# Kernel optimization log

Hardware: AMD Instinct MI355X
Metric: run time of the kernel (lower is better)

Reference implementation:

```python
import jax, jax.numpy as jnp
import numpy as np

VOCAB, X, H, C_CLS = 32000, 300, 512, 5
B, N_LEAVES = 256, 256  # complete binary trees, depth 9, 511 nodes/tree

def setup_inputs() -> dict:
    key = jax.random.key(0)
    ks = jax.random.split(key, 10)
    s = lambda k, shp, fan: jax.random.normal(k, shp, jnp.float32) * (1.0 / np.sqrt(fan))
    return {
        'wordid': jax.random.randint(ks[0], (B, N_LEAVES), 0, VOCAB),
        'emb': jax.random.normal(ks[1], (VOCAB, X), jnp.float32) * 0.1,
        'W_iou_w': s(ks[2], (3 * H, X), X),
        'W_iou_b': jnp.zeros((3 * H,), jnp.float32),
        'U_iou_w': s(ks[3], (3 * H, 2 * H), 2 * H),
        'U_iou_b': jnp.zeros((3 * H,), jnp.float32),
        'U_f_w': s(ks[4], (2 * H, 2 * H), 2 * H),
        'U_f_b': jnp.zeros((2 * H,), jnp.float32),
        'lin_w': s(ks[5], (C_CLS, H), H),
        'lin_b': jnp.zeros((C_CLS,), jnp.float32),
    }

def _cell(iou, c_f):
    i, o, u = jnp.split(iou, 3, axis=-1)
    c = jax.nn.sigmoid(i) * jnp.tanh(u) + c_f
    h = jax.nn.sigmoid(o) * jnp.tanh(c)
    return h, c

def reference(wordid, emb, W_iou_w, W_iou_b, U_iou_w, U_iou_b, U_f_w, U_f_b, lin_w, lin_b):
    b, n = wordid.shape
    # leaves: is_leaf=1 -> iou = W_iou(x), c_f = 0
    x = emb[wordid]                                   # [B, L, X]
    iou = x @ W_iou_w.T + W_iou_b                     # [B, L, 3H]
    h, c = _cell(iou, 0.0)
    hs = [h]
    # internal levels: reduce over exactly 2 children (binary TreeLSTM)
    while h.shape[1] > 1:
        m = h.shape[1] // 2
        h_cat = h.reshape(b, m, 2 * H)                # concat of 2 children
        c_pair = c.reshape(b, m, 2, H)
        f = jax.nn.sigmoid(h_cat @ U_f_w.T + U_f_b).reshape(b, m, 2, H)
        c_f = jnp.sum(f * c_pair, axis=2)             # [B, m, H]
        iou = h_cat @ U_iou_w.T + U_iou_b             # is_leaf=0 branch
        h, c = _cell(iou, c_f)
        hs.append(h)
    h_all = jnp.concatenate(hs, axis=1)               # [B, 2L-1, H], leaves-first topo order
    # dropout is identity at inference
    logits = h_all @ lin_w.T + lin_b                  # [B, 2L-1, num_classes]
    return logits
```

## Files before the change

### kernel.cpp

```cpp
#include <hip/hip_runtime.h>
#include <hip/hip_bf16.h>


typedef __bf16 bf16;
typedef bf16  bf16x8 __attribute__((ext_vector_type(8)));
typedef float f32x4  __attribute__((ext_vector_type(4)));

__device__ __forceinline__ float sigm(float x){ return 1.0f/(1.0f + __expf(-x)); }
__device__ __forceinline__ float tanh_f(float x){ return 1.0f - 2.0f/(__expf(2.0f*x)+1.0f); }

__device__ __forceinline__ void gload16(const bf16* g, bf16* l){
  __builtin_amdgcn_global_load_lds(
      (const __attribute__((address_space(1))) void*)g,
      (__attribute__((address_space(3))) void*)l, 16, 0, 0);
}

__global__ void cvt_all(const float* __restrict__ Wiou, const float* __restrict__ Uiou,
                        const float* __restrict__ Uf, const float* __restrict__ emb,
                        bf16* __restrict__ Wpad, bf16* __restrict__ Uall,
                        bf16* __restrict__ embp){
  const int b = blockIdx.x, t = threadIdx.x;
  if (b < 1536){
    Wpad[b*320 + t] = (bf16)(t < 300 ? Wiou[b*300 + t] : 0.f);
  } else if (b < 1536 + 32000){
    const int r = b - 1536;
    embp[(size_t)r*320 + t] = (bf16)(t < 300 ? emb[(size_t)r*300 + t] : 0.f);
  } else {
    const size_t i = (size_t)(b - 33536)*320 + t;
    if (i < (size_t)1536*1024) Uall[i] = (bf16)Uiou[i];
    else                       Uall[i] = (bf16)Uf[i - (size_t)1536*1024];
  }
}

__global__ __launch_bounds__(256, 2)
void leaf128_kernel(const int* __restrict__ wordid, const bf16* __restrict__ embp,
                    const bf16* __restrict__ Wpad, const float* __restrict__ Wb,
                    bf16* __restrict__ hcur, float* __restrict__ ccur)
{
  __shared__ bf16 lsA[2][128*32];
  __shared__ bf16 lsB[2][192*32];
  const int t = threadIdx.x;
  const int mrow0 = blockIdx.x*128, nblk = blockIdx.y*64;
  const int lane16 = t&15, quad = (t&63)>>4, w = t>>6;

  const int lrow = t>>2;
  const int qsw  = ((t&3) ^ ((t>>3)&3))*8;
  const int wb   = (t & 192)*8;

  const int wid0 = wordid[mrow0 + lrow];
  const int wid1 = wordid[mrow0 + 64 + lrow];
  const bf16* srcA0 = embp + (size_t)wid0*320 + qsw;
  const bf16* srcA1 = embp + (size_t)wid1*320 + qsw;
  const bf16* srcB0 = Wpad + (size_t)(0*512 + nblk + lrow)*320 + qsw;
  const bf16* srcB1 = Wpad + (size_t)(1*512 + nblk + lrow)*320 + qsw;
  const bf16* srcB2 = Wpad + (size_t)(2*512 + nblk + lrow)*320 + qsw;

  const int sA   = (t>>1)&3;
  const int aoff = lane16*32 + ((quad ^ sA)*8);
  const int boff = (w*16 + lane16)*32 + ((quad ^ sA)*8);

  f32x4 acc[3][8];
  const f32x4 zero = {0.f,0.f,0.f,0.f};
  #pragma unroll
  for(int o=0;o<3;o++){
    #pragma unroll
    for(int rt=0;rt<8;rt++) acc[o][rt]=zero;
  }

  {
    bf16* dA = lsA[0]; bf16* dB = lsB[0];
    gload16(srcA0, dA + wb);
    gload16(srcA1, dA + 2048 + wb);
    gload16(srcB0, dB + wb);
    gload16(srcB1, dB + 2048 + wb);
    gload16(srcB2, dB + 4096 + wb);
  }
  __syncthreads();
  int cur = 0;
  for (int ks = 0; ks < 10; ks++){
    if (ks < 9){
      const int k0 = (ks+1)*32;
      bf16* dA = lsA[cur^1]; bf16* dB = lsB[cur^1];
      gload16(srcA0 + k0, dA + wb);
      gload16(srcA1 + k0, dA + 2048 + wb);
      gload16(srcB0 + k0, dB + wb);
      gload16(srcB1 + k0, dB + 2048 + wb);
      gload16(srcB2 + k0, dB + 4096 + wb);
    }
    bf16x8 bfrag[3];
    #pragma unroll
    for(int g=0;g<3;g++) bfrag[g] = *(const bf16x8*)&lsB[cur][g*2048 + boff];
    #pragma unroll
    for(int rt=0;rt<8;rt++){
      bf16x8 a = *(const bf16x8*)&lsA[cur][rt*512 + aoff];
      #pragma unroll
      for(int g=0;g<3;g++)
        acc[g][rt] = __builtin_amdgcn_mfma_f32_16x16x32_bf16(a, bfrag[g], acc[g][rt], 0,0,0);
    }
    __syncthreads();
    cur ^= 1;
  }
  const int j = nblk + w*16 + lane16;
  const float bi=Wb[j], bo=Wb[512+j], bu=Wb[1024+j];
  #pragma unroll
  for(int rt=0;rt<8;rt++){
    #pragma unroll
    for(int reg=0;reg<4;reg++){
      const int row = mrow0 + rt*16 + quad*4 + reg;
      float iv=acc[0][rt][reg]+bi, ov=acc[1][rt][reg]+bo, uv=acc[2][rt][reg]+bu;
      float c = sigm(iv)*tanh_f(uv);
      float h = sigm(ov)*tanh_f(c);
      ccur[(size_t)row*512 + j] = c;
      hcur[(size_t)row*512 + j] = (bf16)h;
    }
  }
}

__global__ __launch_bounds__(256)
void level_kernel(const bf16* __restrict__ hprev, bf16* __restrict__ hcur,
                  const float* __restrict__ cprev, float* __restrict__ ccur,
                  const bf16* __restrict__ Uall, const float* __restrict__ Uioub,
                  const float* __restrict__ Ufb)
{
  __shared__ bf16 lsA[64*40];
  __shared__ bf16 lsB[5][64*40];
  const int t = threadIdx.x;
  const int mrow0 = blockIdx.x*64, nblk = blockIdx.y*64;
  const int r = t>>2, kc = (t&3)*8;
  const int lane16 = t&15, quad = (t&63)>>4, w = t>>6;

  f32x4 acc[5][4];
  const f32x4 zero = {0.f,0.f,0.f,0.f};
  #pragma unroll
  for(int o=0;o<5;o++){
    #pragma unroll
    for(int rt=0;rt<4;rt++) acc[o][rt]=zero;
  }

  const bf16* arow = hprev + (size_t)(mrow0 + r)*1024;
  const int col = nblk + r;
  for (int k0=0;k0<1024;k0+=32){
    *(bf16x8*)&lsA[r*40+kc] = *(const bf16x8*)&arow[k0+kc];
    #pragma unroll
    for(int g=0;g<5;g++)
      *(bf16x8*)&lsB[g][r*40+kc] = *(const bf16x8*)&Uall[(size_t)(g*512+col)*1024 + k0+kc];
    __syncthreads();
    bf16x8 bfrag[5];
    #pragma unroll
    for(int o=0;o<5;o++) bfrag[o] = *(const bf16x8*)&lsB[o][(w*16+lane16)*40 + quad*8];
    #pragma unroll
    for(int rt=0;rt<4;rt++){
      bf16x8 a = *(const bf16x8*)&lsA[(rt*16+lane16)*40 + quad*8];
      #pragma unroll
      for(int o=0;o<5;o++)
        acc[o][rt] = __builtin_amdgcn_mfma_f32_16x16x32_bf16(a, bfrag[o], acc[o][rt], 0,0,0);
    }
    __syncthreads();
  }
  const int j = nblk + w*16 + lane16;
  const float bi =Uioub[j], bo=Uioub[512+j], bu=Uioub[1024+j];
  const float bfl=Ufb[j],   bfr=Ufb[512+j];
  #pragma unroll
  for(int rt=0;rt<4;rt++){
    #pragma unroll
    for(int reg=0;reg<4;reg++){
      const int row = mrow0 + rt*16 + quad*4 + reg;
      float iv=acc[0][rt][reg]+bi, ov=acc[1][rt][reg]+bo, uv=acc[2][rt][reg]+bu;
      float fl=acc[3][rt][reg]+bfl, fr=acc[4][rt][reg]+bfr;
      float cl = cprev[((size_t)row*2  )*512 + j];
      float cr = cprev[((size_t)row*2+1)*512 + j];
      float cf = sigm(fl)*cl + sigm(fr)*cr;
      float c  = sigm(iv)*tanh_f(uv) + cf;
      float h  = sigm(ov)*tanh_f(c);
      ccur[(size_t)row*512 + j] = c;
      hcur[(size_t)row*512 + j] = (bf16)h;
    }
  }
}

__global__ __launch_bounds__(256, 2)
void level128_kernel(const bf16* __restrict__ hprev, bf16* __restrict__ hcur,
                     const float* __restrict__ cprev, float* __restrict__ ccur,
                     const bf16* __restrict__ Uall, const float* __restrict__ Uioub,
                     const float* __restrict__ Ufb)
{
  __shared__ bf16 lsA[2][128*32];
  __shared__ bf16 lsB[2][320*32];
  const int t = threadIdx.x;
  const int mrow0 = blockIdx.x*128, nblk = blockIdx.y*64;
  const int lane16 = t&15, quad = (t&63)>>4, w = t>>6;

  const int lrow = t>>2;
  const int qsw  = ((t&3) ^ ((t>>3)&3))*8;
  const int wb   = (t & 192)*8;

  const bf16* srcA0 = hprev + (size_t)(mrow0 + lrow)*1024 + qsw;
  const bf16* srcA1 = hprev + (size_t)(mrow0 + 64 + lrow)*1024 + qsw;
  const bf16* srcB0 = Uall + (size_t)(0*512 + nblk + lrow)*1024 + qsw;
  const bf16* srcB1 = Uall + (size_t)(1*512 + nblk + lrow)*1024 + qsw;
  const bf16* srcB2 = Uall + (size_t)(2*512 + nblk + lrow)*1024 + qsw;
  const bf16* srcB3 = Uall + (size_t)(3*512 + nblk + lrow)*1024 + qsw;
  const bf16* srcB4 = Uall + (size_t)(4*512 + nblk + lrow)*1024 + qsw;

  const int sA   = (t>>1)&3;
  const int aoff = lane16*32 + ((quad ^ sA)*8);
  const int boff = (w*16 + lane16)*32 + ((quad ^ sA)*8);

  f32x4 acc[5][8];
  const f32x4 zero = {0.f,0.f,0.f,0.f};
  #pragma unroll
  for(int o=0;o<5;o++){
    #pragma unroll
    for(int rt=0;rt<8;rt++) acc[o][rt]=zero;
  }

  {
    bf16* dA = lsA[0]; bf16* dB = lsB[0];
    gload16(srcA0, dA + wb);
    gload16(srcA1, dA + 2048 + wb);
    gload16(srcB0, dB + wb);
    gload16(srcB1, dB + 2048 + wb);
    gload16(srcB2, dB + 4096 + wb);
    gload16(srcB3, dB + 6144 + wb);
    gload16(srcB4, dB + 8192 + wb);
  }
  __syncthreads();
  int cur = 0;
  for (int ks = 0; ks < 32; ks++){
    if (ks < 31){
      const int k0 = (ks+1)*32;
      bf16* dA = lsA[cur^1]; bf16* dB = lsB[cur^1];
      gload16(srcA0 + k0, dA + wb);
      gload16(srcA1 + k0, dA + 2048 + wb);
      gload16(srcB0 + k0, dB + wb);
      gload16(srcB1 + k0, dB + 2048 + wb);
      gload16(srcB2 + k0, dB + 4096 + wb);
      gload16(srcB3 + k0, dB + 6144 + wb);
      gload16(srcB4 + k0, dB + 8192 + wb);
    }
    bf16x8 bfrag[5];
    #pragma unroll
    for(int g=0;g<5;g++) bfrag[g] = *(const bf16x8*)&lsB[cur][g*2048 + boff];
    #pragma unroll
    for(int rt=0;rt<8;rt++){
      bf16x8 a = *(const bf16x8*)&lsA[cur][rt*512 + aoff];
      #pragma unroll
      for(int g=0;g<5;g++)
        acc[g][rt] = __builtin_amdgcn_mfma_f32_16x16x32_bf16(a, bfrag[g], acc[g][rt], 0,0,0);
    }
    __syncthreads();
    cur ^= 1;
  }
  const int j = nblk + w*16 + lane16;
  const float bi =Uioub[j], bo=Uioub[512+j], bu=Uioub[1024+j];
  const float bfl=Ufb[j],   bfr=Ufb[512+j];
  #pragma unroll
  for(int rt=0;rt<8;rt++){
    #pragma unroll
    for(int reg=0;reg<4;reg++){
      const int row = mrow0 + rt*16 + quad*4 + reg;
      float iv=acc[0][rt][reg]+bi, ov=acc[1][rt][reg]+bo, uv=acc[2][rt][reg]+bu;
      float fl=acc[3][rt][reg]+bfl, fr=acc[4][rt][reg]+bfr;
      float cl = cprev[((size_t)row*2  )*512 + j];
      float cr = cprev[((size_t)row*2+1)*512 + j];
      float cf = sigm(fl)*cl + sigm(fr)*cr;
      float c  = sigm(iv)*tanh_f(uv) + cf;
      float h  = sigm(ov)*tanh_f(c);
      ccur[(size_t)row*512 + j] = c;
      hcur[(size_t)row*512 + j] = (bf16)h;
    }
  }
}

__global__ __launch_bounds__(256)
void logits_kernel(const bf16* __restrict__ h, const float* __restrict__ linw,
                   const float* __restrict__ linb, float* __restrict__ out,
                   int rowbase, int lgm, int mask, int off){
  const int row = blockIdx.x*4 + (threadIdx.x>>6);
  const int l = threadIdx.x & 63;
  bf16x8 hv = *(const bf16x8*)(h + (size_t)row*512 + l*8);
  float hf[8];
  #pragma unroll
  for(int jj=0;jj<8;jj++) hf[jj] = (float)hv[jj];
  float s[5];
  #pragma unroll
  for(int c=0;c<5;c++){
    const f32x4 w0 = *(const f32x4*)(linw + c*512 + l*8);
    const f32x4 w1 = *(const f32x4*)(linw + c*512 + l*8 + 4);
    float a = 0.f;
    #pragma unroll
    for(int jj=0;jj<4;jj++) a += hf[jj]*w0[jj] + hf[4+jj]*w1[jj];
    s[c]=a;
  }
  #pragma unroll
  for(int o=32;o>0;o>>=1){
    #pragma unroll
    for(int c=0;c<5;c++) s[c] += __shfl_down(s[c], o, 64);
  }
  if (l==0){
    const int g = rowbase + row;
    const int node = (g>>lgm)*511 + off + (g&mask);
    #pragma unroll
    for(int c=0;c<5;c++) out[(size_t)node*5+c] = s[c] + linb[c];
  }
}

__global__ __launch_bounds__(256)
void logits2_kernel(const bf16* __restrict__ ha, int rows_a, int lgm_a, int mask_a, int off_a,
                    const bf16* __restrict__ hb, int lgm_b, int mask_b, int off_b,
                    const float* __restrict__ linw, const float* __restrict__ linb,
                    float* __restrict__ out){
  const int row = blockIdx.x*4 + (threadIdx.x>>6);
  const int l = threadIdx.x & 63;
  const bf16* hrow; int g, lgm, mask, off;
  if (row < rows_a){ hrow = ha + (size_t)row*512;            g = row;           lgm=lgm_a; mask=mask_a; off=off_a; }
  else             { hrow = hb + (size_t)(row-rows_a)*512;   g = row - rows_a;  lgm=lgm_b; mask=mask_b; off=off_b; }
  bf16x8 hv = *(const bf16x8*)(hrow + l*8);
  float hf[8];
  #pragma unroll
  for(int jj=0;jj<8;jj++) hf[jj] = (float)hv[jj];
  float s[5];
  #pragma unroll
  for(int c=0;c<5;c++){
    const f32x4 w0 = *(const f32x4*)(linw + c*512 + l*8);
    const f32x4 w1 = *(const f32x4*)(linw + c*512 + l*8 + 4);
    float a = 0.f;
    #pragma unroll
    for(int jj=0;jj<4;jj++) a += hf[jj]*w0[jj] + hf[4+jj]*w1[jj];
    s[c]=a;
  }
  #pragma unroll
  for(int o=32;o>0;o>>=1){
    #pragma unroll
    for(int c=0;c<5;c++) s[c] += __shfl_down(s[c], o, 64);
  }
  if (l==0){
    const int node = (g>>lgm)*511 + off + (g&mask);
    #pragma unroll
    for(int c=0;c<5;c++) out[(size_t)node*5+c] = s[c] + linb[c];
  }
}

__global__ void zero_out(float* out, int n){
  int i = blockIdx.x*256 + threadIdx.x;
  if (i < n) out[i] = 0.f;
}

extern "C" void kernel_launch(void* const* d_in, const int* in_sizes, int n_in,
                              void* d_out, int out_size, void* d_ws, size_t ws_size,
                              hipStream_t stream)
{
  const int*   wordid = (const int*)d_in[0];
  const float* emb    = (const float*)d_in[1];
  const float* Wiou   = (const float*)d_in[2];
  const float* Wioub  = (const float*)d_in[3];
  const float* Uiou   = (const float*)d_in[4];
  const float* Uioub  = (const float*)d_in[5];
  const float* Uf     = (const float*)d_in[6];
  const float* Ufb    = (const float*)d_in[7];
  const float* linw   = (const float*)d_in[8];
  const float* linb   = (const float*)d_in[9];
  float* out = (float*)d_out;

  const size_t oWPD  = 0;
  const size_t oUALL = oWPD  + (size_t)1536*320*2;
  const size_t oEMB  = oUALL + (size_t)2560*1024*2;
  const size_t oH1   = oEMB  + (size_t)32000*320*2;
  const size_t oC1   = oH1   + (size_t)32768*512*2;
  const size_t oH0   = oC1   + (size_t)32768*512*4;
  size_t R0 = 0;
  {
    const size_t t2 = oH0 + (size_t)32768*512*(2+4);
    const size_t t4 = oH0 + (size_t)16384*512*(2+4);
    const size_t t8 = oH0 + (size_t) 8192*512*(2+4);
    if      (ws_size >= t2) R0 = 32768;
    else if (ws_size >= t4) R0 = 16384;
    else if (ws_size >= t8) R0 = 8192;
  }
  if (R0 == 0){
    zero_out<<<(out_size+255)/256, 256, 0, stream>>>(out, out_size);
    return;
  }

  char* ws = (char*)d_ws;
  bf16*  Wpad = (bf16*)(ws + oWPD);
  bf16*  Uall = (bf16*)(ws + oUALL);
  bf16*  embp = (bf16*)(ws + oEMB);
  bf16*  h1   = (bf16*)(ws + oH1);
  float* c1   = (float*)(ws + oC1);
  bf16*  h0   = (bf16*)(ws + oH0);
  float* c0   = (float*)(ws + oH0 + R0*1024);

  cvt_all<<<41728, 320, 0, stream>>>(Wiou, Uiou, Uf, emb, Wpad, Uall, embp);

  const int offs[9] = {0,256,384,448,480,496,504,508,510};
  const int nchunk = (int)(65536 / R0);

  for (int ch = 0; ch < nchunk; ch++){
    const int* wid = wordid + (size_t)ch*R0;
    leaf128_kernel<<<dim3((int)(R0/128), 8), 256, 0, stream>>>(wid, embp, Wpad, Wioub,
                                                               h0, c0);
    logits_kernel<<<(int)(R0/4), 256, 0, stream>>>(h0, linw, linb, out,
                                                   (int)(ch*R0), 8, 255, 0);
    bf16*  h1c = h1 + (size_t)ch*(R0/2)*512;
    float* c1c = c1 + (size_t)ch*(R0/2)*512;
    const int orows = (int)(R0/2);
    level128_kernel<<<dim3(orows/128, 8), 256, 0, stream>>>(h0, h1c, c0, c1c,
                                                            Uall, Uioub, Ufb);
  }

  for (int lv = 2; lv <= 8; lv++){
    const int rows = 65536 >> lv;
    const bf16*  hin  = (lv & 1) ? h0 : h1;
    bf16*        hout = (lv & 1) ? h1 : h0;
    const float* cin  = (lv & 1) ? c0 : c1;
    float*       cout = (lv & 1) ? c1 : c0;
    if (rows >= 4096)
      level128_kernel<<<dim3(rows/128, 8), 256, 0, stream>>>(hin, hout, cin, cout,
                                                             Uall, Uioub, Ufb);
    else
      level_kernel<<<dim3(rows/64, 8), 256, 0, stream>>>(hin, hout, cin, cout,
                                                         Uall, Uioub, Ufb);
    if ((lv & 1) == 0){
      const int rows_a = 65536 >> (lv-1);
      const int rows_b = rows;
      logits2_kernel<<<(rows_a + rows_b)/4, 256, 0, stream>>>(
          h1, rows_a, 8-(lv-1), (256>>(lv-1))-1, offs[lv-1],
          h0,         8-lv,     (256>>lv)-1,     offs[lv],
          linw, linb, out);
    }
  }
}
```

Before: 865.2 us.

## Deepen LDS prefetch to two stages with fine-grained waitcnt fences

The leaf and level GEMM kernels now issue loads two K-steps ahead. All LDS fragments are read into registers before a barrier, and the freed buffer is refilled while the MFMAs run under raised priority. Explicit vmcnt/lgkmcnt waits replace the full __syncthreads, so global-to-LDS traffic overlaps compute. The level at 4096 rows now uses the 64-row level_kernel to get more blocks, which trades per-block reuse for occupancy.

```diff
diff --git a/kernel.cpp b/kernel.cpp
--- a/kernel.cpp
+++ b/kernel.cpp
@@ -14,6 +14,13 @@
       (const __attribute__((address_space(1))) void*)g,
       (__attribute__((address_space(3))) void*)l, 16, 0, 0);
 }
+
+#define FENCE_LGKM do{ asm volatile("s_waitcnt lgkmcnt(0)" ::: "memory"); \
+  __builtin_amdgcn_sched_barrier(0); __builtin_amdgcn_s_barrier(); \
+  __builtin_amdgcn_sched_barrier(0); }while(0)
+#define FENCE_VM(N) do{ asm volatile("s_waitcnt vmcnt(" #N ")" ::: "memory"); \
+  __builtin_amdgcn_sched_barrier(0); __builtin_amdgcn_s_barrier(); \
+  __builtin_amdgcn_sched_barrier(0); }while(0)
 
 __global__ void cvt_all(const float* __restrict__ Wiou, const float* __restrict__ Uiou,
                         const float* __restrict__ Uf, const float* __restrict__ emb,
@@ -68,37 +75,39 @@
   }
 
   {
-    bf16* dA = lsA[0]; bf16* dB = lsB[0];
-    gload16(srcA0, dA + wb);
-    gload16(srcA1, dA + 2048 + wb);
-    gload16(srcB0, dB + wb);
-    gload16(srcB1, dB + 2048 + wb);
-    gload16(srcB2, dB + 4096 + wb);
-  }
-  __syncthreads();
-  int cur = 0;
+    gload16(srcA0     , lsA[0] + wb);        gload16(srcA1     , lsA[0] + 2048 + wb);
+    gload16(srcB0     , lsB[0] + wb);        gload16(srcB1     , lsB[0] + 2048 + wb);
+    gload16(srcB2     , lsB[0] + 4096 + wb);
+    gload16(srcA0 + 32, lsA[1] + wb);        gload16(srcA1 + 32, lsA[1] + 2048 + wb);
+    gload16(srcB0 + 32, lsB[1] + wb);        gload16(srcB1 + 32, lsB[1] + 2048 + wb);
+    gload16(srcB2 + 32, lsB[1] + 4096 + wb);
+  }
+  FENCE_VM(5);
+
   for (int ks = 0; ks < 10; ks++){
-    if (ks < 9){
-      const int k0 = (ks+1)*32;
-      bf16* dA = lsA[cur^1]; bf16* dB = lsB[cur^1];
-      gload16(srcA0 + k0, dA + wb);
-      gload16(srcA1 + k0, dA + 2048 + wb);
-      gload16(srcB0 + k0, dB + wb);
-      gload16(srcB1 + k0, dB + 2048 + wb);
-      gload16(srcB2 + k0, dB + 4096 + wb);
-    }
-    bf16x8 bfrag[3];
+    const int cur = ks & 1;
+    bf16x8 bfrag[3], afrag[8];
     #pragma unroll
     for(int g=0;g<3;g++) bfrag[g] = *(const bf16x8*)&lsB[cur][g*2048 + boff];
     #pragma unroll
+    for(int rt=0;rt<8;rt++) afrag[rt] = *(const bf16x8*)&lsA[cur][rt*512 + aoff];
+    FENCE_LGKM;
+    if (ks < 8){
+      const int k0 = (ks+2)*32;
+      gload16(srcA0 + k0, lsA[cur] + wb);        gload16(srcA1 + k0, lsA[cur] + 2048 + wb);
+      gload16(srcB0 + k0, lsB[cur] + wb);        gload16(srcB1 + k0, lsB[cur] + 2048 + wb);
+      gload16(srcB2 + k0, lsB[cur] + 4096 + wb);
+    }
+    __builtin_amdgcn_s_setprio(1);
+    #pragma unroll
     for(int rt=0;rt<8;rt++){
-      bf16x8 a = *(const bf16x8*)&lsA[cur][rt*512 + aoff];
       #pragma unroll
       for(int g=0;g<3;g++)
-        acc[g][rt] = __builtin_amdgcn_mfma_f32_16x16x32_bf16(a, bfrag[g], acc[g][rt], 0,0,0);
-    }
-    __syncthreads();
-    cur ^= 1;
+        acc[g][rt] = __builtin_amdgcn_mfma_f32_16x16x32_bf16(afrag[rt], bfrag[g], acc[g][rt], 0,0,0);
+    }
+    __builtin_amdgcn_s_setprio(0);
+    if (ks < 8)      FENCE_VM(5);
+    else if (ks < 9) FENCE_VM(0);
   }
   const int j = nblk + w*16 + lane16;
   const float bi=Wb[j], bo=Wb[512+j], bu=Wb[1024+j];
@@ -215,41 +224,42 @@
   }
 
   {
-    bf16* dA = lsA[0]; bf16* dB = lsB[0];
-    gload16(srcA0, dA + wb);
-    gload16(srcA1, dA + 2048 + wb);
-    gload16(srcB0, dB + wb);
-    gload16(srcB1, dB + 2048 + wb);
-    gload16(srcB2, dB + 4096 + wb);
-    gload16(srcB3, dB + 6144 + wb);
-    gload16(srcB4, dB + 8192 + wb);
-  }
-  __syncthreads();
-  int cur = 0;
+    gload16(srcA0     , lsA[0] + wb);        gload16(srcA1     , lsA[0] + 2048 + wb);
+    gload16(srcB0     , lsB[0] + wb);        gload16(srcB1     , lsB[0] + 2048 + wb);
+    gload16(srcB2     , lsB[0] + 4096 + wb); gload16(srcB3     , lsB[0] + 6144 + wb);
+    gload16(srcB4     , lsB[0] + 8192 + wb);
+    gload16(srcA0 + 32, lsA[1] + wb);        gload16(srcA1 + 32, lsA[1] + 2048 + wb);
+    gload16(srcB0 + 32, lsB[1] + wb);        gload16(srcB1 + 32, lsB[1] + 2048 + wb);
+    gload16(srcB2 + 32, lsB[1] + 4096 + wb); gload16(srcB3 + 32, lsB[1] + 6144 + wb);
+    gload16(srcB4 + 32, lsB[1] + 8192 + wb);
+  }
+  FENCE_VM(7);
+
   for (int ks = 0; ks < 32; ks++){
-    if (ks < 31){
-      const int k0 = (ks+1)*32;
-      bf16* dA = lsA[cur^1]; bf16* dB = lsB[cur^1];
-      gload16(srcA0 + k0, dA + wb);
-      gload16(srcA1 + k0, dA + 2048 + wb);
-      gload16(srcB0 + k0, dB + wb);
-      gload16(srcB1 + k0, dB + 2048 + wb);
-      gload16(srcB2 + k0, dB + 4096 + wb);
-      gload16(srcB3 + k0, dB + 6144 + wb);
-      gload16(srcB4 + k0, dB + 8192 + wb);
-    }
-    bf16x8 bfrag[5];
+    const int cur = ks & 1;
+    bf16x8 bfrag[5], afrag[8];
     #pragma unroll
     for(int g=0;g<5;g++) bfrag[g] = *(const bf16x8*)&lsB[cur][g*2048 + boff];
     #pragma unroll
+    for(int rt=0;rt<8;rt++) afrag[rt] = *(const bf16x8*)&lsA[cur][rt*512 + aoff];
+    FENCE_LGKM;
+    if (ks < 30){
+      const int k0 = (ks+2)*32;
+      gload16(srcA0 + k0, lsA[cur] + wb);        gload16(srcA1 + k0, lsA[cur] + 2048 + wb);
+      gload16(srcB0 + k0, lsB[cur] + wb);        gload16(srcB1 + k0, lsB[cur] + 2048 + wb);
+      gload16(srcB2 + k0, lsB[cur] + 4096 + wb); gload16(srcB3 + k0, lsB[cur] + 6144 + wb);
+      gload16(srcB4 + k0, lsB[cur] + 8192 + wb);
+    }
+    __builtin_amdgcn_s_setprio(1);
+    #pragma unroll
     for(int rt=0;rt<8;rt++){
-      bf16x8 a = *(const bf16x8*)&lsA[cur][rt*512 + aoff];
       #pragma unroll
       for(int g=0;g<5;g++)
-        acc[g][rt] = __builtin_amdgcn_mfma_f32_16x16x32_bf16(a, bfrag[g], acc[g][rt], 0,0,0);
-    }
-    __syncthreads();
-    cur ^= 1;
+        acc[g][rt] = __builtin_amdgcn_mfma_f32_16x16x32_bf16(afrag[rt], bfrag[g], acc[g][rt], 0,0,0);
+    }
+    __builtin_amdgcn_s_setprio(0);
+    if (ks < 30)      FENCE_VM(7);
+    else if (ks < 31) FENCE_VM(0);
   }
   const int j = nblk + w*16 + lane16;
   const float bi =Uioub[j], bo=Uioub[512+j], bu=Uioub[1024+j];
@@ -415,7 +425,7 @@
     bf16*        hout = (lv & 1) ? h1 : h0;
     const float* cin  = (lv & 1) ? c0 : c1;
     float*       cout = (lv & 1) ? c1 : c0;
-    if (rows >= 4096)
+    if (rows >= 8192)
       level128_kernel<<<dim3(rows/128, 8), 256, 0, stream>>>(hin, hout, cin, cout,
                                                              Uall, Uioub, Ufb);
     else
```

Measured after the change: 846.3 us. 1.02x faster.
